# Optimization experiments

Measured on AMD Instinct MI355X. Metric: run time of the kernel, lower is better.

The kernel has to match this reference:

```python
import jax, jax.numpy as jnp
import numpy as np

NEG_SLOPE = 0.2  # PyG GATv2Conv default leaky_relu slope


def _gatv2(x, src, dst, valid, Wl, bl, Wr, br, att, bias, concat):
    """Faithful PyG GATv2Conv (share_weights=False, add_self_loops=True).
    src/dst already include appended self loops; `valid` masks out original
    self-loop edges (remove_self_loops semantics) with fixed shapes.
    """
    N = x.shape[0]
    H, C = att.shape
    xl = (x @ Wl + bl).reshape(N, H, C)  # source transform
    xr = (x @ Wr + br).reshape(N, H, C)  # destination transform
    xj = xl[src]                          # [Etot,H,C] gathered messages
    e = jax.nn.leaky_relu(xr[dst] + xj, NEG_SLOPE)
    logits = jnp.einsum('ehc,hc->eh', e, att)  # [Etot,H]
    logits = jnp.where(valid[:, None], logits, -jnp.inf)
    # segment softmax over incoming edges of each dst node
    m = jax.ops.segment_max(logits, dst, num_segments=N)          # [N,H]
    m = jnp.where(jnp.isfinite(m), m, 0.0)
    ex = jnp.where(valid[:, None], jnp.exp(logits - m[dst]), 0.0)
    denom = jax.ops.segment_sum(ex, dst, num_segments=N)          # >0 (self loops)
    alpha = ex / denom[dst]                                       # [Etot,H]
    out = jax.ops.segment_sum(alpha[:, :, None] * xj, dst, num_segments=N)
    out = out.reshape(N, H * C) if concat else out.mean(axis=1)
    return out + bias


def _glorot(key, shape):
    fan = shape[0] + shape[-1] if len(shape) > 1 else shape[0]
    return jax.random.normal(key, shape, jnp.float32) * np.sqrt(2.0 / fan)


def setup_inputs() -> dict:
    key = jax.random.key(0)
    ks = jax.random.split(key, 24)
    N, E, F, B, NC = 50000, 800000, 32, 64, 10
    x = jax.random.normal(ks[0], (N, F), jnp.float32)
    edge_index = jax.random.randint(ks[1], (2, E), 0, N, jnp.int64)
    batch_index = jnp.sort(jax.random.randint(ks[2], (N,), 0, B, jnp.int64))
    d = {"x": x, "edge_index": edge_index, "batch_index": batch_index}
    # layer 0: 32 -> 64, heads=3, concat
    d["Wl0"] = _glorot(ks[3], (F, 192)); d["bl0"] = jnp.zeros((192,), jnp.float32)
    d["Wr0"] = _glorot(ks[4], (F, 192)); d["br0"] = jnp.zeros((192,), jnp.float32)
    d["att0"] = _glorot(ks[5], (3, 64)); d["bias0"] = jnp.zeros((192,), jnp.float32)
    # layer 1: 192 -> 64, heads=2, concat
    d["Wl1"] = _glorot(ks[6], (192, 128)); d["bl1"] = jnp.zeros((128,), jnp.float32)
    d["Wr1"] = _glorot(ks[7], (192, 128)); d["br1"] = jnp.zeros((128,), jnp.float32)
    d["att1"] = _glorot(ks[8], (2, 64)); d["bias1"] = jnp.zeros((128,), jnp.float32)
    # layer 2: 128 -> 64, heads=2, mean over heads
    d["Wl2"] = _glorot(ks[9], (128, 128)); d["bl2"] = jnp.zeros((128,), jnp.float32)
    d["Wr2"] = _glorot(ks[10], (128, 128)); d["br2"] = jnp.zeros((128,), jnp.float32)
    d["att2"] = _glorot(ks[11], (2, 64)); d["bias2"] = jnp.zeros((64,), jnp.float32)
    # output linear: 128 -> num_classes
    d["Wout"] = _glorot(ks[12], (128, NC)); d["bout"] = jnp.zeros((NC,), jnp.float32)
    return d


def reference(x, edge_index, batch_index,
              Wl0, bl0, Wr0, br0, att0, bias0,
              Wl1, bl1, Wr1, br1, att1, bias1,
              Wl2, bl2, Wr2, br2, att2, bias2,
              Wout, bout):
    N = x.shape[0]
    B = 64  # number of graphs
    loop = jnp.arange(N, dtype=edge_index.dtype)
    src = jnp.concatenate([edge_index[0], loop])
    dst = jnp.concatenate([edge_index[1], loop])
    valid = jnp.concatenate([edge_index[0] != edge_index[1],
                             jnp.ones((N,), bool)])  # drop accidental self loops

    h = jax.nn.relu(_gatv2(x, src, dst, valid, Wl0, bl0, Wr0, br0, att0, bias0, True))
    h = jax.nn.relu(_gatv2(h, src, dst, valid, Wl1, bl1, Wr1, br1, att1, bias1, True))
    h = jax.nn.relu(_gatv2(h, src, dst, valid, Wl2, bl2, Wr2, br2, att2, bias2, False))

    # global max pool + global mean pool over graphs
    gmx = jax.ops.segment_max(h, batch_index, num_segments=B)
    gmx = jnp.where(jnp.isfinite(gmx), gmx, 0.0)
    cnt = jax.ops.segment_sum(jnp.ones((N,), h.dtype), batch_index, num_segments=B)
    gmn = jax.ops.segment_sum(h, batch_index, num_segments=B) / jnp.maximum(cnt, 1.0)[:, None]
    pooled = jnp.concatenate([gmx, gmn], axis=1)  # [B, 128]
    return pooled @ Wout + bout
```

## Files before the change

### kernel.cpp

```cpp
#include <hip/hip_runtime.h>
#include <hip/hip_bf16.h>
#include <math.h>

#define NEG_SLOPE 0.2f

typedef __attribute__((ext_vector_type(8))) short short8;
typedef __attribute__((ext_vector_type(4))) float f32x4;

__device__ __forceinline__ unsigned short f2b(float v){
    unsigned int b = __float_as_uint(v);
    return (unsigned short)((b + 0x7FFFu + ((b >> 16) & 1u)) >> 16);
}

__device__ __forceinline__ float swz_add16(float p){
    int q;
    q = __builtin_amdgcn_ds_swizzle(__float_as_int(p), 0x041F); p += __int_as_float(q);
    q = __builtin_amdgcn_ds_swizzle(__float_as_int(p), 0x081F); p += __int_as_float(q);
    q = __builtin_amdgcn_ds_swizzle(__float_as_int(p), 0x101F); p += __int_as_float(q);
    q = __builtin_amdgcn_ds_swizzle(__float_as_int(p), 0x201F); p += __int_as_float(q);
    return p;
}


__global__ void edge_count(const int* __restrict__ src, const int* __restrict__ dst,
                           int E, int* __restrict__ counts){
    int e = blockIdx.x * blockDim.x + threadIdx.x;
    if (e >= E) return;
    int s = src[e], d = dst[e];
    if (s != d) atomicAdd(&counts[d], 1);
}

__global__ void scan_block(const int* __restrict__ counts, int* __restrict__ offsets,
                           int* __restrict__ blockSums, int N){
    __shared__ int sh[256];
    int t = threadIdx.x;
    int i = blockIdx.x * 256 + t;
    int v = (i < N) ? counts[i] : 0;
    sh[t] = v; __syncthreads();
    for (int off = 1; off < 256; off <<= 1){
        int x = (t >= off) ? sh[t - off] : 0;
        __syncthreads();
        sh[t] += x;
        __syncthreads();
    }
    if (i < N) offsets[i] = sh[t] - v;
    if (t == 255) blockSums[blockIdx.x] = sh[255];
}

__global__ void scan_sums(int* __restrict__ blockSums, int nb){
    __shared__ int sh[256];
    int t = threadIdx.x;
    int v = (t < nb) ? blockSums[t] : 0;
    sh[t] = v; __syncthreads();
    for (int off = 1; off < 256; off <<= 1){
        int x = (t >= off) ? sh[t - off] : 0;
        __syncthreads();
        sh[t] += x;
        __syncthreads();
    }
    if (t < nb) blockSums[t] = sh[t] - v;
}

__global__ void scan_add(int* __restrict__ offsets, int* __restrict__ cursor,
                         const int* __restrict__ blockSums, int N){
    int i = blockIdx.x * 256 + threadIdx.x;
    if (i < N){
        int v = offsets[i] + blockSums[blockIdx.x];
        offsets[i] = v;
        cursor[i]  = v;
    }
}

__global__ void edge_scatter(const int* __restrict__ src, const int* __restrict__ dst,
                             int E, int* __restrict__ cursor,
                             int* __restrict__ e384, int* __restrict__ e256){
    int e = blockIdx.x * blockDim.x + threadIdx.x;
    if (e >= E) return;
    int s = src[e], d = dst[e];
    if (s != d){
        int pos = atomicAdd(&cursor[d], 1);
        e384[pos] = s * 384;
        e256[pos] = s * 256;
    }
}

__global__ void build_wt_all(const float* __restrict__ Wl0, const float* __restrict__ Wr0,
                             const float* __restrict__ Wl1, const float* __restrict__ Wr1,
                             const float* __restrict__ Wl2, const float* __restrict__ Wr2,
                             unsigned short* __restrict__ WT0,
                             unsigned short* __restrict__ WT1,
                             unsigned short* __restrict__ WT2){
    int i = blockIdx.x * 256 + threadIdx.x;
    if (i < 12288){
        int c = i / 32, k = i - c * 32;
        float v = (c < 192) ? Wl0[(size_t)k * 192 + c] : Wr0[(size_t)k * 192 + (c - 192)];
        WT0[i] = f2b(v);
    } else if (i < 61440){
        int j = i - 12288;
        int c = j / 192, k = j - c * 192;
        float v = (c < 128) ? Wl1[(size_t)k * 128 + c] : Wr1[(size_t)k * 128 + (c - 128)];
        WT1[j] = f2b(v);
    } else if (i < 94208){
        int j = i - 61440;
        int c = j / 128, k = j - c * 128;
        float v = (c < 128) ? Wl2[(size_t)k * 128 + c] : Wr2[(size_t)k * 128 + (c - 128)];
        WT2[j] = f2b(v);
    }
}

template<int K, int COLS, int HC, bool INB>
__global__ __launch_bounds__(256)
void mfma_dual_linear(const void* __restrict__ in_,
                      const unsigned short* __restrict__ WT,
                      const float* __restrict__ bl, const float* __restrict__ br,
                      unsigned short* __restrict__ xlb,
                      float* __restrict__ xr,
                      int N){
    constexpr int KP = K + 8;
    constexpr int CT = COLS / 64;
    __shared__ __align__(16) unsigned short xs[64 * KP];
    __shared__ __align__(16) float ep[4][64 * 20];
    const int tid = threadIdx.x;
    const int row0 = blockIdx.x * 64;

    {
        const int r = tid >> 2, q = tid & 3;
        int gr = row0 + r; if (gr > N - 1) gr = N - 1;
        unsigned short* op = &xs[r * KP + q * (K / 4)];
        if (INB){
            const unsigned short* ip = (const unsigned short*)in_ + (size_t)gr * K + q * (K / 4);
            #pragma unroll
            for (int kk = 0; kk < K / 4; kk += 8)
                *(uint4*)&op[kk] = *(const uint4*)&ip[kk];
        } else {
            const float* ip = (const float*)in_ + (size_t)gr * K + q * (K / 4);
            #pragma unroll
            for (int kk = 0; kk < K / 4; kk += 4){
                float4 v = *(const float4*)&ip[kk];
                ushort4 o;
                o.x = f2b(v.x); o.y = f2b(v.y); o.z = f2b(v.z); o.w = f2b(v.w);
                *(ushort4*)&op[kk] = o;
            }
        }
    }
    __syncthreads();

    const int w = tid >> 6, lane = tid & 63;
    const int lr = lane & 15, lk = (lane >> 4) * 8;

    f32x4 acc[CT][4];
    #pragma unroll
    for (int ct = 0; ct < CT; ++ct){
        int c = (w * CT + ct) * 16 + lr;
        float bv = (c < HC) ? bl[c] : br[c - HC];
        #pragma unroll
        for (int rt = 0; rt < 4; ++rt) acc[ct][rt] = {bv, bv, bv, bv};
    }

    #pragma unroll
    for (int ks = 0; ks < K / 32; ++ks){
        short8 a[4];
        #pragma unroll
        for (int rt = 0; rt < 4; ++rt)
            a[rt] = *(const short8*)&xs[(rt * 16 + lr) * KP + ks * 32 + lk];
        #pragma unroll
        for (int ct = 0; ct < CT; ++ct){
            int c = (w * CT + ct) * 16 + lr;
            short8 b = *(const short8*)&WT[(size_t)c * K + ks * 32 + lk];
            #pragma unroll
            for (int rt = 0; rt < 4; ++rt)
                acc[ct][rt] = __builtin_amdgcn_mfma_f32_16x16x32_bf16(a[rt], b, acc[ct][rt], 0, 0, 0);
        }
    }

    float* my = ep[w];
    const int rb4 = (lane >> 4) * 4;
    #pragma unroll
    for (int ct = 0; ct < CT; ++ct){
        #pragma unroll
        for (int rt = 0; rt < 4; ++rt){
            const int rbase = rt * 16 + rb4;
            #pragma unroll
            for (int r = 0; r < 4; ++r)
                my[(rbase + r) * 20 + lr] = acc[ct][rt][r];
        }
        const int c0 = (w * CT + ct) * 16;
        const bool left = c0 < HC;
        #pragma unroll
        for (int i = 0; i < 4; ++i){
            int chunk = lane + 64 * i;
            int row = chunk >> 2;
            int c4 = (chunk & 3) * 4;
            int grow = row0 + row;
            if (grow < N){
                float4 v = *(float4*)&my[row * 20 + c4];
                if (left){
                    uint2 w2;
                    w2.x = (unsigned)f2b(v.x) | ((unsigned)f2b(v.y) << 16);
                    w2.y = (unsigned)f2b(v.z) | ((unsigned)f2b(v.w) << 16);
                    *(uint2*)&xlb[(size_t)grow * HC + c0 + c4] = w2;
                } else {
                    *(float4*)&xr[(size_t)grow * HC + (c0 - HC) + c4] = v;
                }
            }
        }
    }
}

template<int H, bool MEAN, bool OUTB>
__global__ __launch_bounds__(256)
void gatv2_agg(const unsigned short* __restrict__ xlb, const float* __restrict__ xr,
               const float* __restrict__ att, const float* __restrict__ bias,
               const int* __restrict__ offsets, const int* __restrict__ counts,
               const int* __restrict__ ebyte,
               void* __restrict__ hout, int N){
    const int HC = H * 64;
    const int RB = HC * 2;
    int wid  = (blockIdx.x * 256 + threadIdx.x) >> 6;
    int lane = threadIdx.x & 63;
    int g = lane >> 4, sl = lane & 15, cb = sl * 4;
    int n, h0, h1;
    if (MEAN){ n = wid; h0 = 0; h1 = H; }
    else     { n = wid / H; h0 = wid - n * H; h1 = h0 + 1; }
    if (n >= N) return;
    const int rs = offsets[n];
    const int total = counts[n] + 1;
    const char* XB = (const char*)xlb;
    const unsigned selfb = (unsigned)(n * RB);

    float ox = 0.f, oy = 0.f, oz = 0.f, ow = 0.f;
    for (int h = h0; h < h1; ++h){
        const float4 a4 = *(const float4*)&att[h * 64 + cb];
        const float4 q4 = *(const float4*)&xr[(size_t)n * HC + h * 64 + cb];
        const unsigned colb = (unsigned)((h * 64 + cb) * 2);
        float m = -INFINITY, den = 0.f;
        float ax = 0.f, ay = 0.f, az = 0.f, aw = 0.f;
        int vi = g;
        if (vi < total){
            unsigned boff = (g == 0) ? selfb : (unsigned)ebyte[rs + g - 1];
            uint2 u = *(const uint2*)(XB + (boff + colb));
            unsigned boffn = (unsigned)ebyte[rs + vi + 3];
            while (vi < total){
                int vin = vi + 4;
                uint2 un = *(const uint2*)(XB + (boffn + colb));
                boffn = (unsigned)ebyte[rs + vin + 3];
                float x0 = __uint_as_float(u.x << 16);
                float x1 = __uint_as_float(u.x & 0xFFFF0000u);
                float x2 = __uint_as_float(u.y << 16);
                float x3 = __uint_as_float(u.y & 0xFFFF0000u);
                float t0 = q4.x + x0, t1 = q4.y + x1;
                float t2 = q4.z + x2, t3 = q4.w + x3;
                t0 = fmaxf(t0, NEG_SLOPE * t0);
                t1 = fmaxf(t1, NEG_SLOPE * t1);
                t2 = fmaxf(t2, NEG_SLOPE * t2);
                t3 = fmaxf(t3, NEG_SLOPE * t3);
                float p = a4.x * t0 + a4.y * t1 + a4.z * t2 + a4.w * t3;
                p = swz_add16(p);
                float d = p - m;
                if (d > 8.f){
                    float s = __expf(-d);
                    den *= s; ax *= s; ay *= s; az *= s; aw *= s;
                    m = p; d = 0.f;
                }
                float eb = __expf(d);
                den += eb;
                ax += eb * x0; ay += eb * x1;
                az += eb * x2; aw += eb * x3;
                u = un; vi = vin;
            }
        }
        #pragma unroll
        for (int off = 16; off <= 32; off <<= 1){
            float mo  = __shfl_xor(m,  off, 64);
            float dno = __shfl_xor(den, off, 64);
            float bx = __shfl_xor(ax, off, 64), by = __shfl_xor(ay, off, 64);
            float bz = __shfl_xor(az, off, 64), bw = __shfl_xor(aw, off, 64);
            float Mn = fmaxf(m, mo);
            float sa = (m  == -INFINITY) ? 0.f : __expf(m  - Mn);
            float sb = (mo == -INFINITY) ? 0.f : __expf(mo - Mn);
            den = den * sa + dno * sb;
            ax = ax * sa + bx * sb; ay = ay * sa + by * sb;
            az = az * sa + bz * sb; aw = aw * sa + bw * sb;
            m = Mn;
        }
        float inv = 1.f / den;
        ox += ax * inv; oy += ay * inv; oz += az * inv; ow += aw * inv;
    }
    if (lane < 16){
        if (MEAN){
            const float s = 1.f / H;
            const float4 bv = *(const float4*)&bias[cb];
            float4 o;
            o.x = fmaxf(ox * s + bv.x, 0.f);
            o.y = fmaxf(oy * s + bv.y, 0.f);
            o.z = fmaxf(oz * s + bv.z, 0.f);
            o.w = fmaxf(ow * s + bv.w, 0.f);
            *(float4*)&((float*)hout)[(size_t)n * 64 + cb] = o;
        } else {
            const float4 bv = *(const float4*)&bias[h0 * 64 + cb];
            float o0 = fmaxf(ox + bv.x, 0.f), o1 = fmaxf(oy + bv.y, 0.f);
            float o2 = fmaxf(oz + bv.z, 0.f), o3 = fmaxf(ow + bv.w, 0.f);
            if (OUTB){
                uint2 w2;
                w2.x = (unsigned)f2b(o0) | ((unsigned)f2b(o1) << 16);
                w2.y = (unsigned)f2b(o2) | ((unsigned)f2b(o3) << 16);
                *(uint2*)&((unsigned short*)hout)[(size_t)n * HC + h0 * 64 + cb] = w2;
            } else {
                float4 o; o.x = o0; o.y = o1; o.z = o2; o.w = o3;
                *(float4*)&((float*)hout)[(size_t)n * HC + h0 * 64 + cb] = o;
            }
        }
    }
}

__global__ __launch_bounds__(256)
void pool_kernel(const float* __restrict__ h, const int* __restrict__ batch,
                 int N, float* __restrict__ gmx, float* __restrict__ gsum,
                 int* __restrict__ gcnt){
    const int lane = threadIdx.x & 63;
    const int w = threadIdx.x >> 6;
    const int n0 = blockIdx.x * 256;
    const int nend = min(n0 + 256, N);
    float rmax = 0.f, rsum = 0.f;
    int curG = -1, cnt = 0;
    for (int n = n0 + w; n < nend; n += 4){
        int g = batch[n];
        float v = h[(size_t)n * 64 + lane];
        if (g != curG){
            if (curG >= 0){
                atomicMax((int*)&gmx[curG * 64 + lane], __float_as_int(rmax));
                atomicAdd(&gsum[curG * 64 + lane], rsum);
                if (lane == 0) atomicAdd(&gcnt[curG], cnt);
            }
            curG = g; rmax = v; rsum = v; cnt = 1;
        } else {
            rmax = fmaxf(rmax, v); rsum += v; ++cnt;
        }
    }
    if (curG >= 0){
        atomicMax((int*)&gmx[curG * 64 + lane], __float_as_int(rmax));
        atomicAdd(&gsum[curG * 64 + lane], rsum);
        if (lane == 0) atomicAdd(&gcnt[curG], cnt);
    }
}

__global__ __launch_bounds__(640)
void final_linear(const float* __restrict__ gmx, const float* __restrict__ gsum,
                  const int* __restrict__ gcnt,
                  const float* __restrict__ Wout, const float* __restrict__ bout,
                  float* __restrict__ out){
    __shared__ float sg[4096], ss[4096];
    int t = threadIdx.x;
    for (int i = t; i < 4096; i += 640){ sg[i] = gmx[i]; ss[i] = gsum[i]; }
    __syncthreads();
    int g = t / 10, oc = t % 10;
    float icnt = 1.f / (float)max(gcnt[g], 1);
    float acc = bout[oc], accs = 0.f;
    #pragma unroll 4
    for (int k = 0; k < 64; ++k) acc  += sg[g * 64 + k] * Wout[k * 10 + oc];
    #pragma unroll 4
    for (int k = 0; k < 64; ++k) accs += ss[g * 64 + k] * Wout[(64 + k) * 10 + oc];
    out[g * 10 + oc] = acc + accs * icnt;
}

extern "C" void kernel_launch(void* const* d_in, const int* in_sizes, int n_in,
                              void* d_out, int out_size, void* d_ws, size_t ws_size,
                              hipStream_t stream){
    const int N = 50000, E = 800000, B = 64;
    const float* x    = (const float*)d_in[0];
    const int*  ei    = (const int*)d_in[1];
    const int*  batch = (const int*)d_in[2];
    const float *Wl0=(const float*)d_in[3],  *bl0=(const float*)d_in[4],
                *Wr0=(const float*)d_in[5],  *br0=(const float*)d_in[6],
                *att0=(const float*)d_in[7], *bias0=(const float*)d_in[8];
    const float *Wl1=(const float*)d_in[9],  *bl1=(const float*)d_in[10],
                *Wr1=(const float*)d_in[11], *br1=(const float*)d_in[12],
                *att1=(const float*)d_in[13],*bias1=(const float*)d_in[14];
    const float *Wl2=(const float*)d_in[15], *bl2=(const float*)d_in[16],
                *Wr2=(const float*)d_in[17], *br2=(const float*)d_in[18],
                *att2=(const float*)d_in[19],*bias2=(const float*)d_in[20];
    const float *Wout=(const float*)d_in[21],*bout=(const float*)d_in[22];

    const int* srcA = ei;
    const int* dstA = ei + E;

    char* p = (char*)d_ws;
    auto alloc = [&](size_t bytes)->void*{ void* r = (void*)p; p += (bytes + 255) & ~(size_t)255; return r; };
    void*  bufA   = alloc((size_t)N * 192 * 4);
    float* bufC   = (float*)alloc((size_t)N * 192 * 4);
    unsigned short* xlb = (unsigned short*)alloc((size_t)N * 192 * 2);
    unsigned short* WT0 = (unsigned short*)alloc((size_t)384 * 32 * 2);
    unsigned short* WT1 = (unsigned short*)alloc((size_t)256 * 192 * 2);
    unsigned short* WT2 = (unsigned short*)alloc((size_t)256 * 128 * 2);
    int* counts   = (int*)alloc((size_t)N * 4);
    int* offsets  = (int*)alloc((size_t)N * 4);
    int* cursor   = (int*)alloc((size_t)N * 4);
    int* blockSums= (int*)alloc(256 * 4);
    int* eb384    = (int*)alloc((size_t)(E + 24) * 4);
    int* eb256    = (int*)alloc((size_t)(E + 24) * 4);
    float* pool   = (float*)alloc((size_t)(B * 128 + B) * 4);
    float* gmx  = pool;
    float* gsum = pool + B * 64;
    int*   gcnt = (int*)(pool + B * 128);

    build_wt_all<<<(94208 + 255) / 256, 256, 0, stream>>>(Wl0, Wr0, Wl1, Wr1, Wl2, Wr2, WT0, WT1, WT2);

    hipMemsetAsync(counts, 0, (size_t)N * 4, stream);
    hipMemsetAsync(eb384, 0, (size_t)(E + 24) * 4, stream);
    hipMemsetAsync(eb256, 0, (size_t)(E + 24) * 4, stream);
    int eb = (E + 255) / 256;
    int nb = (N + 255) / 256;
    edge_count<<<eb, 256, 0, stream>>>(srcA, dstA, E, counts);
    scan_block<<<nb, 256, 0, stream>>>(counts, offsets, blockSums, N);
    scan_sums<<<1, 256, 0, stream>>>(blockSums, nb);
    scan_add<<<nb, 256, 0, stream>>>(offsets, cursor, blockSums, N);
    edge_scatter<<<eb, 256, 0, stream>>>(srcA, dstA, E, cursor, eb384, eb256);

    const int rb = (N + 63) / 64;

    mfma_dual_linear<32, 384, 192, false><<<rb, 256, 0, stream>>>(x, WT0, bl0, br0, xlb, bufC, N);
    gatv2_agg<3, false, true><<<(N * 3 + 3) / 4, 256, 0, stream>>>(xlb, bufC, att0, bias0, offsets, counts, eb384, bufA, N);

    mfma_dual_linear<192, 256, 128, true><<<rb, 256, 0, stream>>>(bufA, WT1, bl1, br1, xlb, bufC, N);
    gatv2_agg<2, false, true><<<(N * 2 + 3) / 4, 256, 0, stream>>>(xlb, bufC, att1, bias1, offsets, counts, eb256, bufA, N);

    mfma_dual_linear<128, 256, 128, true><<<rb, 256, 0, stream>>>(bufA, WT2, bl2, br2, xlb, bufC, N);
    gatv2_agg<2, true, false><<<(N + 3) / 4, 256, 0, stream>>>(xlb, bufC, att2, bias2, offsets, counts, eb256, bufA, N);

    hipMemsetAsync(pool, 0, (size_t)(B * 128 + B) * 4, stream);
    pool_kernel<<<(N + 255) / 256, 256, 0, stream>>>((const float*)bufA, batch, N, gmx, gsum, gcnt);
    final_linear<<<1, 640, 0, stream>>>(gmx, gsum, gcnt, Wout, bout, (float*)d_out);
}
```

Baseline: 389.6 us.

## Process all heads per wavefront in GATv2 aggregation and alias GEMM shared memory

The aggregation kernel now assigns one wavefront per destination node that handles every head, instead of one wavefront per (node, head). Each neighbor's edge-index load and offset chase is shared across heads, and the per-head gathers are issued together to raise memory-level parallelism. The cost is more registers per thread and fewer, longer waves. Separately, the linear kernel's input tile and epilogue staging buffer now share one LDS allocation with a barrier between uses, cutting LDS per block to allow higher occupancy.

```diff
diff --git a/kernel.cpp b/kernel.cpp
--- a/kernel.cpp
+++ b/kernel.cpp
@@ -118,8 +118,11 @@
                       int N){
     constexpr int KP = K + 8;
     constexpr int CT = COLS / 64;
-    __shared__ __align__(16) unsigned short xs[64 * KP];
-    __shared__ __align__(16) float ep[4][64 * 20];
+    constexpr int XS_BYTES = 64 * KP * 2;
+    constexpr int EP_BYTES = 4 * 64 * 20 * 4;
+    constexpr int SM_BYTES = XS_BYTES > EP_BYTES ? XS_BYTES : EP_BYTES;
+    __shared__ __align__(16) char smem[SM_BYTES];
+    unsigned short* xs = (unsigned short*)smem;
     const int tid = threadIdx.x;
     const int row0 = blockIdx.x * 64;
 
@@ -173,7 +176,8 @@
         }
     }
 
-    float* my = ep[w];
+    __syncthreads();
+    float* my = ((float*)smem) + w * (64 * 20);
     const int rb4 = (lane >> 4) * 4;
     #pragma unroll
     for (int ct = 0; ct < CT; ++ct){
@@ -216,78 +220,93 @@
                void* __restrict__ hout, int N){
     const int HC = H * 64;
     const int RB = HC * 2;
-    int wid  = (blockIdx.x * 256 + threadIdx.x) >> 6;
+    int n    = (blockIdx.x * 256 + threadIdx.x) >> 6;
     int lane = threadIdx.x & 63;
     int g = lane >> 4, sl = lane & 15, cb = sl * 4;
-    int n, h0, h1;
-    if (MEAN){ n = wid; h0 = 0; h1 = H; }
-    else     { n = wid / H; h0 = wid - n * H; h1 = h0 + 1; }
     if (n >= N) return;
     const int rs = offsets[n];
     const int total = counts[n] + 1;
     const char* XB = (const char*)xlb;
     const unsigned selfb = (unsigned)(n * RB);
 
-    float ox = 0.f, oy = 0.f, oz = 0.f, ow = 0.f;
-    for (int h = h0; h < h1; ++h){
-        const float4 a4 = *(const float4*)&att[h * 64 + cb];
-        const float4 q4 = *(const float4*)&xr[(size_t)n * HC + h * 64 + cb];
-        const unsigned colb = (unsigned)((h * 64 + cb) * 2);
-        float m = -INFINITY, den = 0.f;
-        float ax = 0.f, ay = 0.f, az = 0.f, aw = 0.f;
-        int vi = g;
-        if (vi < total){
-            unsigned boff = (g == 0) ? selfb : (unsigned)ebyte[rs + g - 1];
-            uint2 u = *(const uint2*)(XB + (boff + colb));
-            unsigned boffn = (unsigned)ebyte[rs + vi + 3];
-            while (vi < total){
-                int vin = vi + 4;
-                uint2 un = *(const uint2*)(XB + (boffn + colb));
-                boffn = (unsigned)ebyte[rs + vin + 3];
-                float x0 = __uint_as_float(u.x << 16);
-                float x1 = __uint_as_float(u.x & 0xFFFF0000u);
-                float x2 = __uint_as_float(u.y << 16);
-                float x3 = __uint_as_float(u.y & 0xFFFF0000u);
-                float t0 = q4.x + x0, t1 = q4.y + x1;
-                float t2 = q4.z + x2, t3 = q4.w + x3;
+    float4 a4[H], q4[H];
+    float m[H], den[H], ax[H], ay[H], az[H], aw[H];
+    #pragma unroll
+    for (int h = 0; h < H; ++h){
+        a4[h] = *(const float4*)&att[h * 64 + cb];
+        q4[h] = *(const float4*)&xr[(size_t)n * HC + h * 64 + cb];
+        m[h] = -INFINITY; den[h] = 0.f;
+        ax[h] = 0.f; ay[h] = 0.f; az[h] = 0.f; aw[h] = 0.f;
+    }
+
+    int vi = g;
+    if (vi < total){
+        unsigned boff = (g == 0) ? selfb : (unsigned)ebyte[rs + g - 1];
+        uint2 u[H];
+        #pragma unroll
+        for (int h = 0; h < H; ++h)
+            u[h] = *(const uint2*)(XB + (boff + (unsigned)((h * 64 + cb) * 2)));
+        unsigned boffn = (unsigned)ebyte[rs + vi + 3];
+        while (vi < total){
+            int vin = vi + 4;
+            uint2 un[H];
+            #pragma unroll
+            for (int h = 0; h < H; ++h)
+                un[h] = *(const uint2*)(XB + (boffn + (unsigned)((h * 64 + cb) * 2)));
+            boffn = (unsigned)ebyte[rs + vin + 3];
+            #pragma unroll
+            for (int h = 0; h < H; ++h){
+                float x0 = __uint_as_float(u[h].x << 16);
+                float x1 = __uint_as_float(u[h].x & 0xFFFF0000u);
+                float x2 = __uint_as_float(u[h].y << 16);
+                float x3 = __uint_as_float(u[h].y & 0xFFFF0000u);
+                float t0 = q4[h].x + x0, t1 = q4[h].y + x1;
+                float t2 = q4[h].z + x2, t3 = q4[h].w + x3;
                 t0 = fmaxf(t0, NEG_SLOPE * t0);
                 t1 = fmaxf(t1, NEG_SLOPE * t1);
                 t2 = fmaxf(t2, NEG_SLOPE * t2);
                 t3 = fmaxf(t3, NEG_SLOPE * t3);
-                float p = a4.x * t0 + a4.y * t1 + a4.z * t2 + a4.w * t3;
+                float p = a4[h].x * t0 + a4[h].y * t1 + a4[h].z * t2 + a4[h].w * t3;
                 p = swz_add16(p);
-                float d = p - m;
+                float d = p - m[h];
                 if (d > 8.f){
                     float s = __expf(-d);
-                    den *= s; ax *= s; ay *= s; az *= s; aw *= s;
-                    m = p; d = 0.f;
+                    den[h] *= s; ax[h] *= s; ay[h] *= s; az[h] *= s; aw[h] *= s;
+                    m[h] = p; d = 0.f;
                 }
                 float eb = __expf(d);
-                den += eb;
-                ax += eb * x0; ay += eb * x1;
-                az += eb * x2; aw += eb * x3;
-                u = un; vi = vin;
+                den[h] += eb;
+                ax[h] += eb * x0; ay[h] += eb * x1;
+                az[h] += eb * x2; aw[h] += eb * x3;
+                u[h] = un[h];
             }
-        }
+            vi = vin;
+        }
+    }
+    #pragma unroll
+    for (int h = 0; h < H; ++h){
         #pragma unroll
         for (int off = 16; off <= 32; off <<= 1){
-            float mo  = __shfl_xor(m,  off, 64);
-            float dno = __shfl_xor(den, off, 64);
-            float bx = __shfl_xor(ax, off, 64), by = __shfl_xor(ay, off, 64);
-            float bz = __shfl_xor(az, off, 64), bw = __shfl_xor(aw, off, 64);
-            float Mn = fmaxf(m, mo);
-            float sa = (m  == -INFINITY) ? 0.f : __expf(m  - Mn);
-            float sb = (mo == -INFINITY) ? 0.f : __expf(mo - Mn);
-            den = den * sa + dno * sb;
-            ax = ax * sa + bx * sb; ay = ay * sa + by * sb;
-            az = az * sa + bz * sb; aw = aw * sa + bw * sb;
-            m = Mn;
-        }
-        float inv = 1.f / den;
-        ox += ax * inv; oy += ay * inv; oz += az * inv; ow += aw * inv;
+            float mo  = __shfl_xor(m[h],  off, 64);
+            float dno = __shfl_xor(den[h], off, 64);
+            float bx = __shfl_xor(ax[h], off, 64), by = __shfl_xor(ay[h], off, 64);
+            float bz = __shfl_xor(az[h], off, 64), bw = __shfl_xor(aw[h], off, 64);
+            float Mn = fmaxf(m[h], mo);
+            float sa = (m[h] == -INFINITY) ? 0.f : __expf(m[h] - Mn);
+            float sb = (mo   == -INFINITY) ? 0.f : __expf(mo   - Mn);
+            den[h] = den[h] * sa + dno * sb;
+            ax[h] = ax[h] * sa + bx * sb; ay[h] = ay[h] * sa + by * sb;
+            az[h] = az[h] * sa + bz * sb; aw[h] = aw[h] * sa + bw * sb;
+            m[h] = Mn;
+        }
+        float inv = 1.f / den[h];
+        ax[h] *= inv; ay[h] *= inv; az[h] *= inv; aw[h] *= inv;
     }
     if (lane < 16){
         if (MEAN){
+            float ox = 0.f, oy = 0.f, oz = 0.f, ow = 0.f;
+            #pragma unroll
+            for (int h = 0; h < H; ++h){ ox += ax[h]; oy += ay[h]; oz += az[h]; ow += aw[h]; }
             const float s = 1.f / H;
             const float4 bv = *(const float4*)&bias[cb];
             float4 o;
@@ -297,17 +316,20 @@
             o.w = fmaxf(ow * s + bv.w, 0.f);
             *(float4*)&((float*)hout)[(size_t)n * 64 + cb] = o;
         } else {
-            const float4 bv = *(const float4*)&bias[h0 * 64 + cb];
-            float o0 = fmaxf(ox + bv.x, 0.f), o1 = fmaxf(oy + bv.y, 0.f);
-            float o2 = fmaxf(oz + bv.z, 0.f), o3 = fmaxf(ow + bv.w, 0.f);
-            if (OUTB){
-                uint2 w2;
-                w2.x = (unsigned)f2b(o0) | ((unsigned)f2b(o1) << 16);
-                w2.y = (unsigned)f2b(o2) | ((unsigned)f2b(o3) << 16);
-                *(uint2*)&((unsigned short*)hout)[(size_t)n * HC + h0 * 64 + cb] = w2;
-            } else {
-                float4 o; o.x = o0; o.y = o1; o.z = o2; o.w = o3;
-                *(float4*)&((float*)hout)[(size_t)n * HC + h0 * 64 + cb] = o;
+            #pragma unroll
+            for (int h = 0; h < H; ++h){
+                const float4 bv = *(const float4*)&bias[h * 64 + cb];
+                float o0 = fmaxf(ax[h] + bv.x, 0.f), o1 = fmaxf(ay[h] + bv.y, 0.f);
+                float o2 = fmaxf(az[h] + bv.z, 0.f), o3 = fmaxf(aw[h] + bv.w, 0.f);
+                if (OUTB){
+                    uint2 w2;
+                    w2.x = (unsigned)f2b(o0) | ((unsigned)f2b(o1) << 16);
+                    w2.y = (unsigned)f2b(o2) | ((unsigned)f2b(o3) << 16);
+                    *(uint2*)&((unsigned short*)hout)[(size_t)n * HC + h * 64 + cb] = w2;
+                } else {
+                    float4 o; o.x = o0; o.y = o1; o.z = o2; o.w = o3;
+                    *(float4*)&((float*)hout)[(size_t)n * HC + h * 64 + cb] = o;
+                }
             }
         }
     }
@@ -417,15 +439,16 @@
     edge_scatter<<<eb, 256, 0, stream>>>(srcA, dstA, E, cursor, eb384, eb256);
 
     const int rb = (N + 63) / 64;
+    const int ab = (N + 3) / 4;
 
     mfma_dual_linear<32, 384, 192, false><<<rb, 256, 0, stream>>>(x, WT0, bl0, br0, xlb, bufC, N);
-    gatv2_agg<3, false, true><<<(N * 3 + 3) / 4, 256, 0, stream>>>(xlb, bufC, att0, bias0, offsets, counts, eb384, bufA, N);
+    gatv2_agg<3, false, true><<<ab, 256, 0, stream>>>(xlb, bufC, att0, bias0, offsets, counts, eb384, bufA, N);
 
     mfma_dual_linear<192, 256, 128, true><<<rb, 256, 0, stream>>>(bufA, WT1, bl1, br1, xlb, bufC, N);
-    gatv2_agg<2, false, true><<<(N * 2 + 3) / 4, 256, 0, stream>>>(xlb, bufC, att1, bias1, offsets, counts, eb256, bufA, N);
+    gatv2_agg<2, false, true><<<ab, 256, 0, stream>>>(xlb, bufC, att1, bias1, offsets, counts, eb256, bufA, N);
 
     mfma_dual_linear<128, 256, 128, true><<<rb, 256, 0, stream>>>(bufA, WT2, bl2, br2, xlb, bufC, N);
-    gatv2_agg<2, true, false><<<(N + 3) / 4, 256, 0, stream>>>(xlb, bufC, att2, bias2, offsets, counts, eb256, bufA, N);
+    gatv2_agg<2, true, false><<<ab, 256, 0, stream>>>(xlb, bufC, att2, bias2, offsets, counts, eb256, bufA, N);
 
     hipMemsetAsync(pool, 0, (size_t)(B * 128 + B) * 4, stream);
     pool_kernel<<<(N + 255) / 256, 256, 0, stream>>>((const float*)bufA, batch, N, gmx, gsum, gcnt);
```

Measured after the change: 367.0 us. 5.8% less time.
